# Performance work log

Measured on AMD Instinct MI355X. Metric: run time of the kernel, lower is better.

The kernel has to match this reference:

```python
import jax, jax.numpy as jnp
import numpy as np

B, S, E = 4, 2048, 1024
H = E // 2  # per-head dim (2 heads)


def setup_inputs() -> dict:
    key = jax.random.key(0)
    ks = jax.random.split(key, 10)
    w = 0.02
    return {
        "input": jax.random.normal(ks[0], (B, S, E), dtype=jnp.float32),
        "Wq": jax.random.normal(ks[1], (2, H, H), dtype=jnp.float32) * w,
        "bq": jax.random.normal(ks[2], (2, H), dtype=jnp.float32) * w,
        "Wk": jax.random.normal(ks[3], (2, H, H), dtype=jnp.float32) * w,
        "bk": jax.random.normal(ks[4], (2, H), dtype=jnp.float32) * w,
        "Wv": jax.random.normal(ks[5], (2, H, H), dtype=jnp.float32) * w,
        "bv": jax.random.normal(ks[6], (2, H), dtype=jnp.float32) * w,
        "Wf": jax.random.normal(ks[7], (E, E), dtype=jnp.float32) * w,
        "bf": jax.random.normal(ks[8], (E,), dtype=jnp.float32) * w,
        "masked": 1,
    }


def reference(input, Wq, bq, Wk, bk, Wv, bv, Wf, bf, masked):
    b, s, e = input.shape
    h = e // 2
    # contiguous split into 2 heads: [b, s, 2, h]
    xh = input.reshape(b, s, 2, h)
    # per-head Linear: y = x @ W.T + b  (W is [out, in])
    q = jnp.einsum("bsnh,noh->bsno", xh, Wq) + bq
    k = jnp.einsum("bsnh,noh->bsno", xh, Wk) + bk
    v = jnp.einsum("bsnh,noh->bsno", xh, Wv) + bv
    # scores: [b, n, s, t]
    scores = jnp.einsum("bsno,btno->bnst", q, k) / jnp.sqrt(jnp.float32(h))
    if masked:
        causal = jnp.tril(jnp.ones((s, s), dtype=bool))
        scores = jnp.where(causal, scores, jnp.float32(-jnp.inf))
    probs = jax.nn.softmax(scores, axis=-1)
    out = jnp.einsum("bnst,btnh->bsnh", probs, v).reshape(b, s, e)
    return jnp.einsum("bse,oe->bso", out, Wf) + bf
```

## Files before the change

kernel.cpp:

```cpp
#include <hip/hip_runtime.h>
#include <hip/hip_bf16.h>

#define BB 4
#define SS 2048
#define EE 1024
#define HH 512

typedef __attribute__((ext_vector_type(8))) short short8;
typedef __attribute__((ext_vector_type(4))) float f32x4;
typedef __attribute__((ext_vector_type(16))) float f32x16;

static __device__ __forceinline__ unsigned short f2bf(float x){
  unsigned u = __float_as_uint(x);
  u += 0x7fffu + ((u >> 16) & 1u);
  return (unsigned short)(u >> 16);
}

static __device__ __forceinline__ unsigned cvtpk(float lo, float hi){
  unsigned d;
  asm("v_cvt_pk_bf16_f32 %0, %1, %2" : "=v"(d) : "v"(lo), "v"(hi));
  return d;
}

static __device__ __forceinline__ void gload16(const void* g, void* l){
  __builtin_amdgcn_global_load_lds((const __attribute__((address_space(1))) void*)g,
                                   (__attribute__((address_space(3))) void*)l, 16, 0, 0);
}

__global__ void k_cvt(const float* __restrict__ in, unsigned short* __restrict__ out, int n8){
  int idx = blockIdx.x * blockDim.x + threadIdx.x;
  int stride = gridDim.x * blockDim.x;
  for (int i = idx; i < n8; i += stride){
    const float4* p = (const float4*)in + (long)i * 2;
    float4 a = p[0], b = p[1];
    union { unsigned short u[8]; uint4 v; } r;
    r.u[0]=f2bf(a.x); r.u[1]=f2bf(a.y); r.u[2]=f2bf(a.z); r.u[3]=f2bf(a.w);
    r.u[4]=f2bf(b.x); r.u[5]=f2bf(b.y); r.u[6]=f2bf(b.z); r.u[7]=f2bf(b.w);
    ((uint4*)out)[i] = r.v;
  }
}

#define GBK 32

template<bool OUT_BF16>
static __device__ __forceinline__ void gemm_tile(
    const unsigned short* __restrict__ A, int lda,
    const unsigned short* __restrict__ Bw, int ldb,
    void* __restrict__ Cc, int ldc,
    const float* __restrict__ bias, int K, int row0, int col0, float oscale)
{
  __shared__ unsigned short As[2][128 * GBK];
  __shared__ unsigned short Bs[2][128 * GBK];
  const int tid = threadIdx.x, lane = tid & 63, w = tid >> 6;
  const int wm = w >> 1, wn = w & 1;
  const int fr = lane & 15, g = lane >> 4;

  f32x4 acc[4][4];
  #pragma unroll
  for (int i = 0; i < 4; i++)
    #pragma unroll
    for (int j = 0; j < 4; j++){ acc[i][j][0]=0.f; acc[i][j][1]=0.f; acc[i][j][2]=0.f; acc[i][j][3]=0.f; }

  const unsigned short* gAsrc[2]; const unsigned short* gBsrc[2];
  unsigned ldsOff[2];
  #pragma unroll
  for (int i = 0; i < 2; i++){
    int slot = w*128 + i*64 + lane;
    int row = slot >> 2, ch = slot & 3;
    int sc_ = ch ^ ((row >> 1) & 3);
    gAsrc[i] = A  + (long)(row0 + row) * lda + sc_ * 8;
    gBsrc[i] = Bw + (long)(col0 + row) * ldb + sc_ * 8;
    ldsOff[i] = (unsigned)((w*128 + i*64) * 8);
  }

  unsigned aoff[4], boff[4];
  #pragma unroll
  for (int mi = 0; mi < 4; mi++){
    int row = wm*64 + mi*16 + fr;
    aoff[mi] = row * GBK + ((g ^ ((row >> 1) & 3)) * 8);
  }
  #pragma unroll
  for (int ni = 0; ni < 4; ni++){
    int row = wn*64 + ni*16 + fr;
    boff[ni] = row * GBK + ((g ^ ((row >> 1) & 3)) * 8);
  }

  const int KT = K / GBK;
  #pragma unroll
  for (int i = 0; i < 2; i++) gload16(gAsrc[i], &As[0][ldsOff[i]]);
  #pragma unroll
  for (int i = 0; i < 2; i++) gload16(gBsrc[i], &Bs[0][ldsOff[i]]);
  __syncthreads();

  for (int kt = 0; kt < KT; ++kt){
    const int cur = kt & 1;
    if (kt + 1 < KT){
      #pragma unroll
      for (int i = 0; i < 2; i++) gload16(gAsrc[i] + (kt+1)*GBK, &As[cur^1][ldsOff[i]]);
      #pragma unroll
      for (int i = 0; i < 2; i++) gload16(gBsrc[i] + (kt+1)*GBK, &Bs[cur^1][ldsOff[i]]);
    }
    short8 av[4], bv[4];
    #pragma unroll
    for (int mi = 0; mi < 4; mi++) av[mi] = *(const short8*)&As[cur][aoff[mi]];
    #pragma unroll
    for (int ni = 0; ni < 4; ni++) bv[ni] = *(const short8*)&Bs[cur][boff[ni]];
    #pragma unroll
    for (int mi = 0; mi < 4; mi++)
      #pragma unroll
      for (int ni = 0; ni < 4; ni++)
        acc[mi][ni] = __builtin_amdgcn_mfma_f32_16x16x32_bf16(av[mi], bv[ni], acc[mi][ni], 0, 0, 0);
    __syncthreads();
  }

  #pragma unroll
  for (int mi = 0; mi < 4; mi++){
    #pragma unroll
    for (int ni = 0; ni < 4; ni++){
      int row = row0 + wm*64 + mi*16 + g*4;
      int col = col0 + wn*64 + ni*16 + fr;
      float bb = bias[col];
      #pragma unroll
      for (int r = 0; r < 4; r++){
        float v = (acc[mi][ni][r] + bb) * oscale;
        if (OUT_BF16) ((unsigned short*)Cc)[(long)(row + r) * ldc + col] = f2bf(v);
        else          ((float*)Cc)[(long)(row + r) * ldc + col] = v;
      }
    }
  }
}

__global__ __launch_bounds__(256, 2) void k_qkv(
    const unsigned short* __restrict__ xb,
    const unsigned short* __restrict__ wq, const unsigned short* __restrict__ wk,
    const unsigned short* __restrict__ wv,
    const float* __restrict__ bq, const float* __restrict__ bk, const float* __restrict__ bv,
    unsigned short* __restrict__ Q, unsigned short* __restrict__ K, unsigned short* __restrict__ V)
{
  int z = blockIdx.z; int which = z >> 3; int bn = z & 7; int b = bn >> 1, n = bn & 1;
  const unsigned short* W; const float* bias; unsigned short* out;
  float os = 1.f;
  if (which == 0){ W = wq; bias = bq; out = Q; os = 0.044194173824159216f; }
  else if (which == 1){ W = wk; bias = bk; out = K; }
  else { W = wv; bias = bv; out = V; }
  W += n * HH * HH; bias += n * HH; out += (long)bn * SS * HH;
  const unsigned short* Ap = xb + (long)b * SS * EE + n * HH;
  gemm_tile<true>(Ap, EE, W, HH, out, HH, bias, HH, blockIdx.x * 128, blockIdx.y * 128, os);
}

__global__ __launch_bounds__(256, 2) void k_outproj(
    const unsigned short* __restrict__ O, const unsigned short* __restrict__ wf,
    const float* __restrict__ bfb, float* __restrict__ out)
{
  gemm_tile<false>(O, EE, wf, EE, out, EE, bfb, EE, blockIdx.x * 128, blockIdx.y * 128, 1.f);
}

__global__ __launch_bounds__(256) void k_transpose(const unsigned short* __restrict__ V,
                                                   unsigned short* __restrict__ Vt){
  __shared__ unsigned short t[64 * 64];
  long base = (long)blockIdx.z * SS * HH;
  const unsigned short* in = V + base;
  unsigned short* out = Vt + base;
  int s0 = blockIdx.x * 64, o0 = blockIdx.y * 64;
  int tid = threadIdx.x;
  int r = tid >> 3, cch = tid & 7;
  #pragma unroll
  for (int p = 0; p < 2; p++){
    int s = p * 32 + r;
    uint4 v = *(const uint4*)&in[(long)(s0 + s) * HH + o0 + cch * 8];
    *(uint4*)&t[s * 64 + ((cch ^ ((s >> 3) & 7)) * 8)] = v;
  }
  __syncthreads();
  #pragma unroll
  for (int p = 0; p < 2; p++){
    int o = p * 32 + r;
    union { unsigned short u[8]; uint4 v; } x;
    #pragma unroll
    for (int j = 0; j < 8; j++){
      int s = cch * 8 + j;
      x.u[j] = t[s * 64 + (((o >> 3) ^ ((s >> 3) & 7)) * 8) + (o & 7)];
    }
    *(uint4*)&out[(long)(o0 + o) * SS + s0 + cch * 8] = x.v;
  }
}

#define QB 128
#define TB 32

__global__ __launch_bounds__(512, 1) void k_flash7(
    const unsigned short* __restrict__ Qg, const unsigned short* __restrict__ Kg,
    const unsigned short* __restrict__ Vtg,
    unsigned short* __restrict__ Opart, float* __restrict__ mlg,
    const int* __restrict__ maskedp)
{
  __shared__ unsigned short Ks[2][TB * HH];
  __shared__ unsigned short Vs[HH * TB];
  __shared__ float2 Sx[4][2][8][64];

  const int bid = blockIdx.x;
  const int bn = bid & 7;
  const int u = bid >> 3;
  const int masked = *maskedp;
  int qi, c;
  if (masked){
    qi = -1; c = 0;
    int cnt = 0;
    #pragma unroll 1
    for (int q = 0; q < 16; q++){
      int nch = (4*q + 25) / 22;
      if (qi < 0 && u >= cnt && u < cnt + nch){ qi = q; c = u - cnt; }
      cnt += nch;
    }
    if (qi < 0) return;
  } else { qi = u >> 1; c = u & 1; }
  const int n  = masked ? 4*qi + 4 : 64;
  const int CH = masked ? 22 : 32;
  const int t0 = c * CH;
  const int t1 = min(n, t0 + CH);

  const long base = (long)bn * SS * HH;
  const unsigned short* Qp = Qg + base;
  const unsigned short* Kp = Kg + base;
  const unsigned short* Vp = Vtg + base;

  const int tid = threadIdx.x, lane = tid & 63, w = tid >> 6;
  const int ln = lane & 31, hi = lane >> 5;
  const int rg = w & 3, dh = w >> 2;
  const int q0 = qi * QB;
  const int myq = q0 + rg * 32 + ln;

  short8 Qr[16];
  {
    const unsigned short* qrow = Qp + (long)myq * HH + dh * 256 + hi * 8;
    #pragma unroll
    for (int ks = 0; ks < 16; ks++) Qr[ks] = *(const short8*)(qrow + ks * 16);
  }

  f32x16 oa[8];
  #pragma unroll
  for (int i = 0; i < 8; i++)
    #pragma unroll
    for (int r = 0; r < 16; r++) oa[i][r] = 0.f;
  float m_r = -1e30f, l_r = 0.f;

  auto stageK = [&](int buf, int t){
    if (w < 4){
      #pragma unroll
      for (int i = 0; i < 8; i++){
        const int sbase = w * 512 + i * 64;
        const int slot = sbase + lane;
        int row = slot >> 6, ch = slot & 63;
        int sc_ = ch ^ (row & 7);
        gload16(Kp + (long)(t * TB + row) * HH + sc_ * 8, &Ks[buf][sbase * 8]);
      }
    }
  };
  auto stageV = [&](int t){
    if (w >= 4){
      #pragma unroll
      for (int i = 0; i < 8; i++){
        const int sbase = (w - 4) * 512 + i * 64;
        const int slot = sbase + lane;
        int row = slot >> 2, ch = slot & 3;
        int sc_ = ch ^ ((row >> 1) & 3);
        gload16(Vp + (long)row * SS + t * TB + sc_ * 8, &Vs[sbase * 8]);
      }
    }
  };

  stageK(0, t0);
  stageV(t0);
  __syncthreads();

  for (int t = t0; t < t1; ++t){
    const int cur = (t - t0) & 1;
    if (t > t0)     stageV(t);
    if (t + 1 < t1) stageK(cur ^ 1, t + 1);

    f32x16 sa;
    #pragma unroll
    for (int r = 0; r < 16; r++) sa[r] = 0.f;
    #pragma unroll
    for (int ks = 0; ks < 16; ks++){
      int ch = (dh * 32 + ks * 2 + hi) ^ (ln & 7);
      short8 kf = *(const short8*)&Ks[cur][ln * HH + ch * 8];
      sa = __builtin_amdgcn_mfma_f32_32x32x16_bf16(kf, Qr[ks], sa, 0, 0, 0);
    }

    #pragma unroll
    for (int i = 0; i < 8; i++)
      Sx[rg][dh][i][lane] = make_float2(sa[2*i], sa[2*i+1]);

    __syncthreads();

    float p[16];
    #pragma unroll
    for (int i = 0; i < 8; i++){
      float2 o = Sx[rg][dh ^ 1][i][lane];
      p[2*i]   = sa[2*i]   + o.x;
      p[2*i+1] = sa[2*i+1] + o.y;
    }

    if (masked && (t * TB + TB - 1 > myq)){
      #pragma unroll
      for (int r = 0; r < 16; r++){
        int tl = (r & 3) + 8 * (r >> 2) + 4 * hi;
        if (t * TB + tl > myq) p[r] = -1e30f;
      }
    }

    float mx = p[0];
    #pragma unroll
    for (int r = 1; r < 16; r++) mx = fmaxf(mx, p[r]);
    mx = fmaxf(mx, __shfl_xor(mx, 32, 64));
    if (__any(mx > m_r + 8.f)){
      float mn = fmaxf(m_r, mx);
      float alpha = __expf(m_r - mn);
      m_r = mn; l_r *= alpha;
      #pragma unroll
      for (int r = 0; r < 16; r++){
        float al = __shfl(alpha, (r & 3) + 8 * (r >> 2) + 4 * hi, 64);
        #pragma unroll
        for (int i = 0; i < 8; i++) oa[i][r] *= al;
      }
    }
    float ps = 0.f;
    #pragma unroll
    for (int r = 0; r < 16; r++){ float pe = __expf(p[r] - m_r); p[r] = pe; ps += pe; }
    ps += __shfl_xor(ps, 32, 64);
    l_r += ps;

    unsigned W[8], R[8];
    #pragma unroll
    for (int i = 0; i < 8; i++) W[i] = cvtpk(p[2*i], p[2*i+1]);
    #pragma unroll
    for (int i = 0; i < 8; i++) R[i] = __shfl_xor(W[i], 32, 64);
    union { unsigned u[4]; short8 s; } fa0, fa1;
    fa0.u[0] = hi ? R[2] : W[0];  fa0.u[1] = hi ? R[3] : W[1];
    fa0.u[2] = hi ? W[2] : R[0];  fa0.u[3] = hi ? W[3] : R[1];
    fa1.u[0] = hi ? R[6] : W[4];  fa1.u[1] = hi ? R[7] : W[5];
    fa1.u[2] = hi ? W[6] : R[4];  fa1.u[3] = hi ? W[7] : R[5];

    #pragma unroll
    for (int cf = 0; cf < 8; cf++){
      int h = dh * 256 + cf * 32 + ln;
      int sw = (h >> 1) & 3;
      short8 v0 = *(const short8*)&Vs[h * TB + ((hi     ^ sw) * 8)];
      oa[cf] = __builtin_amdgcn_mfma_f32_32x32x16_bf16(fa0.s, v0, oa[cf], 0, 0, 0);
      short8 v1 = *(const short8*)&Vs[h * TB + (((2+hi) ^ sw) * 8)];
      oa[cf] = __builtin_amdgcn_mfma_f32_32x32x16_bf16(fa1.s, v1, oa[cf], 0, 0, 0);
    }

    __syncthreads();
  }

  const long slot = (long)(bn * 16 + qi) * 3 + c;
  unsigned short* dst = Opart + slot * (QB * HH);
  #pragma unroll
  for (int cf = 0; cf < 8; cf++){
    int col = dh * 256 + cf * 32 + ln;
    #pragma unroll
    for (int r = 0; r < 16; r++){
      int row = rg * 32 + (r & 3) + 8 * (r >> 2) + 4 * hi;
      dst[row * HH + col] = f2bf(oa[cf][r]);
    }
  }
  if (w < 4 && hi == 0){
    mlg[slot * 256 + rg * 32 + ln]       = m_r;
    mlg[slot * 256 + 128 + rg * 32 + ln] = l_r;
  }
}

__global__ __launch_bounds__(256) void k_combine(
    const unsigned short* __restrict__ Opart, const float* __restrict__ mlg,
    unsigned short* __restrict__ O, const int* __restrict__ maskedp)
{
  __shared__ float wl[128][3];
  const int gq = blockIdx.x;
  const int bn = gq & 7, qi = gq >> 3;
  const int b = bn >> 1, n = bn & 1;
  const int NC = (*maskedp) ? (4*qi + 25) / 22 : 2;
  const long slotbase = (long)(bn * 16 + qi) * 3;
  const int tid = threadIdx.x;

  if (tid < 128){
    float mc[3], lc[3];
    float M = -1e30f;
    for (int c = 0; c < NC; c++){
      mc[c] = mlg[(slotbase + c) * 256 + tid];
      lc[c] = mlg[(slotbase + c) * 256 + 128 + tid];
      M = fmaxf(M, mc[c]);
    }
    float L = 0.f;
    for (int c = 0; c < NC; c++){
      float wc = __expf(mc[c] - M);
      mc[c] = wc;
      L += lc[c] * wc;
    }
    float inv = 1.f / L;
    #pragma unroll
    for (int c = 0; c < 3; c++) wl[tid][c] = (c < NC) ? mc[c] * inv : 0.f;
  }
  __syncthreads();

  for (int it = 0; it < 32; it++){
    int idx = it * 256 + tid;
    int row = idx >> 6, cv = idx & 63;
    float acc[8] = {0.f,0.f,0.f,0.f,0.f,0.f,0.f,0.f};
    for (int c = 0; c < NC; c++){
      float wc = wl[row][c];
      short8 v = *(const short8*)&Opart[(slotbase + c) * (QB * HH) + row * HH + cv * 8];
      #pragma unroll
      for (int j = 0; j < 8; j++){
        float f = __uint_as_float((unsigned)(unsigned short)v[j] << 16);
        acc[j] += f * wc;
      }
    }
    union { unsigned short u[8]; uint4 q; } rr;
    #pragma unroll
    for (int j = 0; j < 8; j++) rr.u[j] = f2bf(acc[j]);
    long dstoff = ((long)b * SS + qi * QB + row) * EE + n * HH + cv * 8;
    *(uint4*)&O[dstoff] = rr.q;
  }
}

extern "C" void kernel_launch(void* const* d_in, const int* in_sizes, int n_in,
                              void* d_out, int out_size, void* d_ws, size_t ws_size,
                              hipStream_t stream)
{
  const float* x   = (const float*)d_in[0];
  const float* Wq  = (const float*)d_in[1];
  const float* bq  = (const float*)d_in[2];
  const float* Wk  = (const float*)d_in[3];
  const float* bk  = (const float*)d_in[4];
  const float* Wv  = (const float*)d_in[5];
  const float* bv  = (const float*)d_in[6];
  const float* Wf  = (const float*)d_in[7];
  const float* bf_ = (const float*)d_in[8];
  const int* masked = (const int*)d_in[9];

  char* p = (char*)d_ws;
  const long TEN = (long)BB * SS * EE * 2;
  unsigned short* xb  = (unsigned short*)p; p += TEN;
  unsigned short* Qb  = (unsigned short*)p; p += TEN;
  unsigned short* Kb  = (unsigned short*)p; p += TEN;
  unsigned short* Vb  = (unsigned short*)p; p += TEN;
  unsigned short* wqb = (unsigned short*)p; p += 2L * HH * HH * 2;
  unsigned short* wkb = (unsigned short*)p; p += 2L * HH * HH * 2;
  unsigned short* wvb = (unsigned short*)p; p += 2L * HH * HH * 2;
  unsigned short* wfb = (unsigned short*)p; p += (long)EE * EE * 2;
  unsigned short* Opart = (unsigned short*)p; p += 384L * QB * HH * 2;
  float* mlg = (float*)p; p += 384L * 256 * 4;

  k_cvt<<<dim3(2048), 256, 0, stream>>>(x,  xb,  BB * SS * EE / 8);
  k_cvt<<<dim3(256),  256, 0, stream>>>(Wq, wqb, 2 * HH * HH / 8);
  k_cvt<<<dim3(256),  256, 0, stream>>>(Wk, wkb, 2 * HH * HH / 8);
  k_cvt<<<dim3(256),  256, 0, stream>>>(Wv, wvb, 2 * HH * HH / 8);
  k_cvt<<<dim3(512),  256, 0, stream>>>(Wf, wfb, EE * EE / 8);

  k_qkv<<<dim3(SS / 128, HH / 128, 24), 256, 0, stream>>>(xb, wqb, wkb, wvb, bq, bk, bv, Qb, Kb, Vb);
  k_transpose<<<dim3(SS / 64, HH / 64, 8), 256, 0, stream>>>(Vb, xb);
  k_flash7<<<dim3(256), 512, 0, stream>>>(Qb, Kb, xb, Opart, mlg, masked);
  k_combine<<<dim3(128), 256, 0, stream>>>(Opart, mlg, Vb, masked);
  k_outproj<<<dim3((BB * SS) / 128, EE / 128, 1), 256, 0, stream>>>(Vb, wfb, bf_, (float*)d_out);
}
```

Measured before the change: 237.8 us.

## Fuse conversions, write V transposed from GEMM, move K prefetch after sync

The five fp32-to-bf16 conversion launches become one kernel that dispatches on index range. The V projection is split into its own GEMM whose epilogue transposes through LDS and writes V^T directly, so the separate transpose kernel goes away. In the flash kernel the cross-wave score exchange uses float4 instead of float2, and the next K tile is staged after the barrier instead of before the QK MFMAs. This cuts launches and global round trips but adds LDS use to the V GEMM epilogue and changes the timing of the K prefetch.

New measurement: 265.3 us. 11.5% more time.

```diff
diff --git a/kernel.cpp b/kernel.cpp
--- a/kernel.cpp
+++ b/kernel.cpp
@@ -9,6 +9,7 @@
 typedef __attribute__((ext_vector_type(8))) short short8;
 typedef __attribute__((ext_vector_type(4))) float f32x4;
 typedef __attribute__((ext_vector_type(16))) float f32x16;
+typedef __attribute__((ext_vector_type(4))) unsigned short us4;
 
 static __device__ __forceinline__ unsigned short f2bf(float x){
   unsigned u = __float_as_uint(x);
@@ -27,22 +28,38 @@
                                    (__attribute__((address_space(3))) void*)l, 16, 0, 0);
 }
 
-__global__ void k_cvt(const float* __restrict__ in, unsigned short* __restrict__ out, int n8){
+__global__ void k_cvt_all(const float* __restrict__ x,  const float* __restrict__ wq,
+                          const float* __restrict__ wk, const float* __restrict__ wv,
+                          const float* __restrict__ wf,
+                          unsigned short* __restrict__ xb,  unsigned short* __restrict__ wqb,
+                          unsigned short* __restrict__ wkb, unsigned short* __restrict__ wvb,
+                          unsigned short* __restrict__ wfb){
+  const int N0 = 1048576;
+  const int N1 = N0 + 65536;
+  const int N2 = N1 + 65536;
+  const int N3 = N2 + 65536;
+  const int N4 = N3 + 131072;
   int idx = blockIdx.x * blockDim.x + threadIdx.x;
   int stride = gridDim.x * blockDim.x;
-  for (int i = idx; i < n8; i += stride){
-    const float4* p = (const float4*)in + (long)i * 2;
+  for (int i = idx; i < N4; i += stride){
+    const float* src; unsigned short* dst; int j;
+    if (i < N0){ src = x;  dst = xb;  j = i; }
+    else if (i < N1){ src = wq; dst = wqb; j = i - N0; }
+    else if (i < N2){ src = wk; dst = wkb; j = i - N1; }
+    else if (i < N3){ src = wv; dst = wvb; j = i - N2; }
+    else            { src = wf; dst = wfb; j = i - N3; }
+    const float4* p = (const float4*)src + (long)j * 2;
     float4 a = p[0], b = p[1];
     union { unsigned short u[8]; uint4 v; } r;
     r.u[0]=f2bf(a.x); r.u[1]=f2bf(a.y); r.u[2]=f2bf(a.z); r.u[3]=f2bf(a.w);
     r.u[4]=f2bf(b.x); r.u[5]=f2bf(b.y); r.u[6]=f2bf(b.z); r.u[7]=f2bf(b.w);
-    ((uint4*)out)[i] = r.v;
+    ((uint4*)dst)[j] = r.v;
   }
 }
 
 #define GBK 32
 
-template<bool OUT_BF16>
+template<int OUTMODE>
 static __device__ __forceinline__ void gemm_tile(
     const unsigned short* __restrict__ A, int lda,
     const unsigned short* __restrict__ Bw, int ldb,
@@ -113,18 +130,43 @@
     __syncthreads();
   }
 
-  #pragma unroll
-  for (int mi = 0; mi < 4; mi++){
-    #pragma unroll
-    for (int ni = 0; ni < 4; ni++){
-      int row = row0 + wm*64 + mi*16 + g*4;
-      int col = col0 + wn*64 + ni*16 + fr;
-      float bb = bias[col];
-      #pragma unroll
-      for (int r = 0; r < 4; r++){
-        float v = (acc[mi][ni][r] + bb) * oscale;
-        if (OUT_BF16) ((unsigned short*)Cc)[(long)(row + r) * ldc + col] = f2bf(v);
-        else          ((float*)Cc)[(long)(row + r) * ldc + col] = v;
+  if constexpr (OUTMODE == 2){
+    __shared__ unsigned short Ct[128][136];
+    #pragma unroll
+    for (int mi = 0; mi < 4; mi++){
+      #pragma unroll
+      for (int ni = 0; ni < 4; ni++){
+        int rowb = wm*64 + mi*16 + g*4;
+        int col  = wn*64 + ni*16 + fr;
+        float bb = bias[col0 + col];
+        us4 pk;
+        #pragma unroll
+        for (int r = 0; r < 4; r++) pk[r] = f2bf((acc[mi][ni][r] + bb) * oscale);
+        *(us4*)&Ct[col][rowb] = pk;
+      }
+    }
+    __syncthreads();
+    #pragma unroll
+    for (int it = 0; it < 8; it++){
+      int idx2 = it * 256 + tid;
+      int o = idx2 >> 4, sch = idx2 & 15;
+      uint4 v = *(const uint4*)&Ct[o][sch * 8];
+      *(uint4*)&((unsigned short*)Cc)[(long)(col0 + o) * ldc + row0 + sch * 8] = v;
+    }
+  } else {
+    #pragma unroll
+    for (int mi = 0; mi < 4; mi++){
+      #pragma unroll
+      for (int ni = 0; ni < 4; ni++){
+        int row = row0 + wm*64 + mi*16 + g*4;
+        int col = col0 + wn*64 + ni*16 + fr;
+        float bb = bias[col];
+        #pragma unroll
+        for (int r = 0; r < 4; r++){
+          float v = (acc[mi][ni][r] + bb) * oscale;
+          if (OUTMODE == 1) ((unsigned short*)Cc)[(long)(row + r) * ldc + col] = f2bf(v);
+          else              ((float*)Cc)[(long)(row + r) * ldc + col] = v;
+        }
       }
     }
   }
@@ -133,61 +175,42 @@
 __global__ __launch_bounds__(256, 2) void k_qkv(
     const unsigned short* __restrict__ xb,
     const unsigned short* __restrict__ wq, const unsigned short* __restrict__ wk,
-    const unsigned short* __restrict__ wv,
-    const float* __restrict__ bq, const float* __restrict__ bk, const float* __restrict__ bv,
-    unsigned short* __restrict__ Q, unsigned short* __restrict__ K, unsigned short* __restrict__ V)
+    const float* __restrict__ bq, const float* __restrict__ bk,
+    unsigned short* __restrict__ Q, unsigned short* __restrict__ K)
 {
   int z = blockIdx.z; int which = z >> 3; int bn = z & 7; int b = bn >> 1, n = bn & 1;
   const unsigned short* W; const float* bias; unsigned short* out;
   float os = 1.f;
   if (which == 0){ W = wq; bias = bq; out = Q; os = 0.044194173824159216f; }
-  else if (which == 1){ W = wk; bias = bk; out = K; }
-  else { W = wv; bias = bv; out = V; }
+  else { W = wk; bias = bk; out = K; }
   W += n * HH * HH; bias += n * HH; out += (long)bn * SS * HH;
   const unsigned short* Ap = xb + (long)b * SS * EE + n * HH;
-  gemm_tile<true>(Ap, EE, W, HH, out, HH, bias, HH, blockIdx.x * 128, blockIdx.y * 128, os);
+  gemm_tile<1>(Ap, EE, W, HH, out, HH, bias, HH, blockIdx.x * 128, blockIdx.y * 128, os);
+}
+
+__global__ __launch_bounds__(256, 2) void k_qkv_v(
+    const unsigned short* __restrict__ xb, const unsigned short* __restrict__ wv,
+    const float* __restrict__ bv, unsigned short* __restrict__ Vt)
+{
+  int bn = blockIdx.z; int b = bn >> 1, n = bn & 1;
+  const unsigned short* W = wv + n * HH * HH;
+  const float* bias = bv + n * HH;
+  unsigned short* out = Vt + (long)bn * SS * HH;
+  const unsigned short* Ap = xb + (long)b * SS * EE + n * HH;
+  gemm_tile<2>(Ap, EE, W, HH, out, SS, bias, HH, blockIdx.x * 128, blockIdx.y * 128, 1.f);
 }
 
 __global__ __launch_bounds__(256, 2) void k_outproj(
     const unsigned short* __restrict__ O, const unsigned short* __restrict__ wf,
     const float* __restrict__ bfb, float* __restrict__ out)
 {
-  gemm_tile<false>(O, EE, wf, EE, out, EE, bfb, EE, blockIdx.x * 128, blockIdx.y * 128, 1.f);
-}
-
-__global__ __launch_bounds__(256) void k_transpose(const unsigned short* __restrict__ V,
-                                                   unsigned short* __restrict__ Vt){
-  __shared__ unsigned short t[64 * 64];
-  long base = (long)blockIdx.z * SS * HH;
-  const unsigned short* in = V + base;
-  unsigned short* out = Vt + base;
-  int s0 = blockIdx.x * 64, o0 = blockIdx.y * 64;
-  int tid = threadIdx.x;
-  int r = tid >> 3, cch = tid & 7;
-  #pragma unroll
-  for (int p = 0; p < 2; p++){
-    int s = p * 32 + r;
-    uint4 v = *(const uint4*)&in[(long)(s0 + s) * HH + o0 + cch * 8];
-    *(uint4*)&t[s * 64 + ((cch ^ ((s >> 3) & 7)) * 8)] = v;
-  }
-  __syncthreads();
-  #pragma unroll
-  for (int p = 0; p < 2; p++){
-    int o = p * 32 + r;
-    union { unsigned short u[8]; uint4 v; } x;
-    #pragma unroll
-    for (int j = 0; j < 8; j++){
-      int s = cch * 8 + j;
-      x.u[j] = t[s * 64 + (((o >> 3) ^ ((s >> 3) & 7)) * 8) + (o & 7)];
-    }
-    *(uint4*)&out[(long)(o0 + o) * SS + s0 + cch * 8] = x.v;
-  }
+  gemm_tile<0>(O, EE, wf, EE, out, EE, bfb, EE, blockIdx.x * 128, blockIdx.y * 128, 1.f);
 }
 
 #define QB 128
 #define TB 32
 
-__global__ __launch_bounds__(512, 1) void k_flash7(
+__global__ __launch_bounds__(512, 1) void k_flash8(
     const unsigned short* __restrict__ Qg, const unsigned short* __restrict__ Kg,
     const unsigned short* __restrict__ Vtg,
     unsigned short* __restrict__ Opart, float* __restrict__ mlg,
@@ -195,7 +218,7 @@
 {
   __shared__ unsigned short Ks[2][TB * HH];
   __shared__ unsigned short Vs[HH * TB];
-  __shared__ float2 Sx[4][2][8][64];
+  __shared__ float4 Sx[4][2][4][64];
 
   const int bid = blockIdx.x;
   const int bn = bid & 7;
@@ -274,8 +297,7 @@
 
   for (int t = t0; t < t1; ++t){
     const int cur = (t - t0) & 1;
-    if (t > t0)     stageV(t);
-    if (t + 1 < t1) stageK(cur ^ 1, t + 1);
+    if (t > t0) stageV(t);
 
     f32x16 sa;
     #pragma unroll
@@ -288,17 +310,21 @@
     }
 
     #pragma unroll
-    for (int i = 0; i < 8; i++)
-      Sx[rg][dh][i][lane] = make_float2(sa[2*i], sa[2*i+1]);
+    for (int ip = 0; ip < 4; ip++)
+      Sx[rg][dh][ip][lane] = make_float4(sa[4*ip], sa[4*ip+1], sa[4*ip+2], sa[4*ip+3]);
 
     __syncthreads();
 
+    if (t + 1 < t1) stageK(cur ^ 1, t + 1);
+
     float p[16];
     #pragma unroll
-    for (int i = 0; i < 8; i++){
-      float2 o = Sx[rg][dh ^ 1][i][lane];
-      p[2*i]   = sa[2*i]   + o.x;
-      p[2*i+1] = sa[2*i+1] + o.y;
+    for (int ip = 0; ip < 4; ip++){
+      float4 o = Sx[rg][dh ^ 1][ip][lane];
+      p[4*ip]   = sa[4*ip]   + o.x;
+      p[4*ip+1] = sa[4*ip+1] + o.y;
+      p[4*ip+2] = sa[4*ip+2] + o.z;
+      p[4*ip+3] = sa[4*ip+3] + o.w;
     }
 
     if (masked && (t * TB + TB - 1 > myq)){
@@ -444,7 +470,8 @@
   unsigned short* xb  = (unsigned short*)p; p += TEN;
   unsigned short* Qb  = (unsigned short*)p; p += TEN;
   unsigned short* Kb  = (unsigned short*)p; p += TEN;
-  unsigned short* Vb  = (unsigned short*)p; p += TEN;
+  unsigned short* Vt  = (unsigned short*)p; p += TEN;
+  unsigned short* Ob  = (unsigned short*)p; p += TEN;
   unsigned short* wqb = (unsigned short*)p; p += 2L * HH * HH * 2;
   unsigned short* wkb = (unsigned short*)p; p += 2L * HH * HH * 2;
   unsigned short* wvb = (unsigned short*)p; p += 2L * HH * HH * 2;
@@ -452,15 +479,10 @@
   unsigned short* Opart = (unsigned short*)p; p += 384L * QB * HH * 2;
   float* mlg = (float*)p; p += 384L * 256 * 4;
 
-  k_cvt<<<dim3(2048), 256, 0, stream>>>(x,  xb,  BB * SS * EE / 8);
-  k_cvt<<<dim3(256),  256, 0, stream>>>(Wq, wqb, 2 * HH * HH / 8);
-  k_cvt<<<dim3(256),  256, 0, stream>>>(Wk, wkb, 2 * HH * HH / 8);
-  k_cvt<<<dim3(256),  256, 0, stream>>>(Wv, wvb, 2 * HH * HH / 8);
-  k_cvt<<<dim3(512),  256, 0, stream>>>(Wf, wfb, EE * EE / 8);
-
-  k_qkv<<<dim3(SS / 128, HH / 128, 24), 256, 0, stream>>>(xb, wqb, wkb, wvb, bq, bk, bv, Qb, Kb, Vb);
-  k_transpose<<<dim3(SS / 64, HH / 64, 8), 256, 0, stream>>>(Vb, xb);
-  k_flash7<<<dim3(256), 512, 0, stream>>>(Qb, Kb, xb, Opart, mlg, masked);
-  k_combine<<<dim3(128), 256, 0, stream>>>(Opart, mlg, Vb, masked);
-  k_outproj<<<dim3((BB * SS) / 128, EE / 128, 1), 256, 0, stream>>>(Vb, wfb, bf_, (float*)d_out);
-}
+  k_cvt_all<<<dim3(2048), 256, 0, stream>>>(x, Wq, Wk, Wv, Wf, xb, wqb, wkb, wvb, wfb);
+  k_qkv   <<<dim3(SS / 128, HH / 128, 16), 256, 0, stream>>>(xb, wqb, wkb, bq, bk, Qb, Kb);
+  k_qkv_v <<<dim3(SS / 128, HH / 128, 8),  256, 0, stream>>>(xb, wvb, bv, Vt);
+  k_flash8<<<dim3(256), 512, 0, stream>>>(Qb, Kb, Vt, Opart, mlg, masked);
+  k_combine<<<dim3(128), 256, 0, stream>>>(Opart, mlg, Ob, masked);
+  k_outproj<<<dim3((BB * SS) / 128, EE / 128, 1), 256, 0, stream>>>(Ob, wfb, bf_, (float*)d_out);
+}
```
